# Optimization experiments

Hardware: AMD Instinct MI355X
Metric: run time of the kernel (lower is better)

Reference implementation:

```python
import jax, jax.numpy as jnp
import numpy as np

TAU = 0.01
WEIGHT = 1.0
N = 4096


def _isotonic_nondecreasing(y):
    """L2 isotonic regression: argmin_{v_1<=...<=v_n} ||v-y||^2, via the
    min-max formula v_i = max_{j<=i} min_{k>=i} mean(y[j..k]). O(n^2) but fully
    vectorized; the vjp reproduces the block-averaging Jacobian of PAV."""
    n = y.shape[0]
    cs = jnp.concatenate([jnp.zeros((1,), y.dtype), jnp.cumsum(y)])
    j = jnp.arange(n)[:, None]
    k = jnp.arange(n)[None, :]
    M = (cs[k + 1] - cs[j]) / (k - j + 1).astype(y.dtype)  # mean(y[j..k]) for j<=k
    big = jnp.asarray(jnp.inf, y.dtype)
    M = jnp.where(j <= k, M, big)
    # S[j,i] = min_{k>=i} M[j,k]  (reverse cummin along k)
    S = jax.lax.cummin(M[:, ::-1], axis=1)[:, ::-1]
    S = jnp.where(j <= k, S, -big)  # invalidate j>i before cummax over j
    T = jax.lax.cummax(S, axis=0)   # T[i,i] = max_{j<=i} S[j,i]
    return jnp.diagonal(T)


def _soft_rank(values, reg):
    """Differentiable ascending ranks via L2 projection onto the permutahedron
    of w=[n,...,1] (Blondel et al. / torchsort soft_rank, l2 regularization)."""
    n = values.shape[0]
    s_scaled = values / reg
    perm = jnp.argsort(-s_scaled)            # descending order
    s = s_scaled[perm]
    w = jnp.arange(n, 0, -1, dtype=values.dtype)
    v = -_isotonic_nondecreasing(-(s - w))
    primal = s - v
    inv = jnp.argsort(perm)
    return primal[inv]


def _soft_perm(x, tau):
    """Row-stochastic soft permutation: P[i,j] = softmax_j(-(sort(x)_i - x_j)^2/tau).
    As tau->0, P@y reorders y by ascending x."""
    xs = jnp.sort(x)
    logits = -((xs[:, None] - x[None, :]) ** 2) / tau  # [n, n]
    return jax.nn.softmax(logits, axis=-1)


def setup_inputs() -> dict:
    key = jax.random.key(0)
    k1, k2 = jax.random.split(key)
    preds = jax.random.normal(k1, (N,), dtype=jnp.float32)
    target = jax.random.normal(k2, (N,), dtype=jnp.float32)
    return {"preds": preds, "target": target}


def reference(preds, target):
    n = preds.shape[0]
    P = _soft_perm(preds, TAU)               # [n, n]
    y_sorted = P @ target                    # target soft-reordered by preds
    r_sorted = _soft_rank(y_sorted, TAU)     # soft ranks of reordered target
    diff_sum = jnp.abs(r_sorted[1:] - r_sorted[:-1]).sum()
    xi_soft = 1.0 - 3.0 * diff_sum / (n * n - 1)
    loss = -WEIGHT * xi_soft
    return loss, jax.lax.stop_gradient(xi_soft)
```

## Files before the change

kernel.cpp:

```cpp
#include <hip/hip_runtime.h>
#include <hip/hip_bf16.h>
#include <math.h>

#define N 4096


__global__ __launch_bounds__(1024, 4)
void k_A(const float* __restrict__ preds, const float* __restrict__ target,
         float* __restrict__ y) {
    __shared__ __align__(16) float4 sp4[N / 4];
    __shared__ __align__(16) float4 st4[N / 4];
    int tid = threadIdx.x;
    int b = blockIdx.x;
    int lane = tid & 63, wid = tid >> 6;
    const float4* gp = (const float4*)preds;
    const float4* gt = (const float4*)target;
    sp4[tid] = gp[tid];
    st4[tid] = gt[tid];
    __syncthreads();
    const float* sp = (const float*)sp4;
    int i0 = b * 16 + wid;
    float xv = sp[i0];
    float Z = 0.f, Nm = 0.f;
    int cnt = 0;
    #pragma unroll 4
    for (int m = 0; m < 16; m++) {
        int q = lane + 64 * m;
        float4 p4 = sp4[q];
        float4 t4 = st4[q];
        int j = q * 4;
        float d0 = xv - p4.x, d1 = xv - p4.y, d2 = xv - p4.z, d3 = xv - p4.w;
        float e0 = __expf(-100.0f * d0 * d0);
        float e1 = __expf(-100.0f * d1 * d1);
        float e2 = __expf(-100.0f * d2 * d2);
        float e3 = __expf(-100.0f * d3 * d3);
        Z += (e0 + e1) + (e2 + e3);
        Nm += e0 * t4.x + e1 * t4.y + e2 * t4.z + e3 * t4.w;
        cnt += (p4.x < xv) || (p4.x == xv && (j + 0) < i0);
        cnt += (p4.y < xv) || (p4.y == xv && (j + 1) < i0);
        cnt += (p4.z < xv) || (p4.z == xv && (j + 2) < i0);
        cnt += (p4.w < xv) || (p4.w == xv && (j + 3) < i0);
    }
    #pragma unroll
    for (int d = 32; d; d >>= 1) {
        Z += __shfl_down(Z, d);
        Nm += __shfl_down(Nm, d);
        cnt += __shfl_down(cnt, d);
    }
    if (lane == 0) y[cnt] = Nm / Z;
}

__global__ __launch_bounds__(1024, 4)
void k_B(const float* __restrict__ y, float* __restrict__ s_out,
         int* __restrict__ perm_out) {
    __shared__ __align__(16) float sy[N];
    __shared__ int part[16][65];
    int tid = threadIdx.x;
    int b = blockIdx.x;
    ((float4*)sy)[tid] = ((const float4*)y)[tid];
    __syncthreads();
    int eloc = tid & 15;
    int slice = tid >> 4;
    int i = b * 16 + eloc;
    float v = sy[i];
    int cnt = 0;
    const float4* sy4 = (const float4*)sy;
    #pragma unroll
    for (int it = 0; it < 16; it++) {
        int q = slice * 16 + ((it + slice) & 15);
        float4 a = sy4[q];
        int j = q * 4;
        cnt += (a.x > v) || (a.x == v && (j + 0) < i);
        cnt += (a.y > v) || (a.y == v && (j + 1) < i);
        cnt += (a.z > v) || (a.z == v && (j + 2) < i);
        cnt += (a.w > v) || (a.w == v && (j + 3) < i);
    }
    part[eloc][slice] = cnt;
    __syncthreads();
    if (tid < 16) {
        int r = 0;
        #pragma unroll
        for (int q = 0; q < 64; q++) r += part[tid][q];
        int i2 = b * 16 + tid;
        s_out[r] = sy[i2] * 100.0f;
        perm_out[r] = i2;
    }
}

__global__ __launch_bounds__(512, 2)
void k_C(const float* __restrict__ s, float* __restrict__ P) {
    __shared__ __align__(16) float mArr[4][512];
    __shared__ float incl[4][513];
    __shared__ double cj[16];
    __shared__ double wsum[8];
    int tid = threadIdx.x;
    int b = blockIdx.x;
    int j0 = b * 16;
    int kbase = tid * 8;
    int lane = tid & 63, wid = tid >> 6;
    double loc[8];
    {
        const float4* s4 = (const float4*)s;
        double tot = 0.0;
        #pragma unroll
        for (int q = 0; q < 2; q++) {
            float4 a = s4[tid * 2 + q];
            int t0 = kbase + q * 4;
            tot += (double)(N - (t0 + 0)) - (double)a.x; loc[q * 4 + 0] = tot;
            tot += (double)(N - (t0 + 1)) - (double)a.y; loc[q * 4 + 1] = tot;
            tot += (double)(N - (t0 + 2)) - (double)a.z; loc[q * 4 + 2] = tot;
            tot += (double)(N - (t0 + 3)) - (double)a.w; loc[q * 4 + 3] = tot;
        }
        double w = tot;
        #pragma unroll
        for (int d = 1; d < 64; d <<= 1) {
            double o = __shfl_up(w, d);
            if (lane >= d) w += o;
        }
        if (lane == 63) wsum[wid] = w;
        __syncthreads();
        double base = 0.0;
        #pragma unroll
        for (int q = 0; q < 8; q++) if (q < wid) base += wsum[q];
        double excl = base + (w - tot);
        #pragma unroll
        for (int e = 0; e < 8; e++) loc[e] += excl;
        if (tid == 2 * b) {
            cj[0] = excl;
            #pragma unroll
            for (int m = 1; m < 8; m++) cj[m] = loc[m - 1];
        }
        if (tid == 2 * b + 1) {
            cj[8] = excl;
            #pragma unroll
            for (int m = 1; m < 8; m++) cj[8 + m] = loc[m - 1];
        }
    }
    __syncthreads();
    float vloc[8];
    #pragma unroll
    for (int e = 0; e < 8; e++) vloc[e] = -INFINITY;
    float ls[4][8];
    bool live = (tid >= 2 * b);
    for (int grp = 0; grp < 4; grp++) {
        if (live) {
            #pragma unroll
            for (int rq = 0; rq < 4; rq++) {
                int j = j0 + grp * 4 + rq;
                double csj = cj[grp * 4 + rq];
                float run = INFINITY;
                #pragma unroll
                for (int e = 7; e >= 0; e--) {
                    int k = kbase + e;
                    float f = INFINITY;
                    if (k >= j) f = (float)(loc[e] - csj) * __builtin_amdgcn_rcpf((float)(k - j + 1));
                    run = fminf(f, run);
                    ls[rq][e] = run;
                }
                mArr[rq][tid] = run;
            }
        } else {
            #pragma unroll
            for (int rq = 0; rq < 4; rq++) mArr[rq][tid] = INFINITY;
        }
        __syncthreads();
        if (wid < 4) {
            const float4* mv = (const float4*)mArr[wid];
            float4 x0 = mv[2 * lane + 0];
            float4 x1 = mv[2 * lane + 1];
            float s7 = x1.w;
            float s6 = fminf(x1.z, s7);
            float s5 = fminf(x1.y, s6);
            float s4 = fminf(x1.x, s5);
            float s3 = fminf(x0.w, s4);
            float s2 = fminf(x0.z, s3);
            float s1 = fminf(x0.y, s2);
            float s0 = fminf(x0.x, s1);
            float t = s0;
            #pragma unroll
            for (int d = 1; d < 64; d <<= 1) {
                float o = __shfl_down(t, d);
                if (lane + d < 64) t = fminf(t, o);
            }
            float after = __shfl_down(t, 1);
            if (lane == 63) after = INFINITY;
            incl[wid][8 * lane + 0] = fminf(s0, after);
            incl[wid][8 * lane + 1] = fminf(s1, after);
            incl[wid][8 * lane + 2] = fminf(s2, after);
            incl[wid][8 * lane + 3] = fminf(s3, after);
            incl[wid][8 * lane + 4] = fminf(s4, after);
            incl[wid][8 * lane + 5] = fminf(s5, after);
            incl[wid][8 * lane + 6] = fminf(s6, after);
            incl[wid][8 * lane + 7] = fminf(s7, after);
            if (lane == 0) incl[wid][512] = INFINITY;
        }
        __syncthreads();
        if (live) {
            #pragma unroll
            for (int rq = 0; rq < 4; rq++) {
                int j = j0 + grp * 4 + rq;
                float aft = incl[rq][tid + 1];
                #pragma unroll
                for (int e = 0; e < 8; e++) {
                    int i = kbase + e;
                    float sv = fminf(ls[rq][e], aft);
                    if (i >= j) vloc[e] = fmaxf(vloc[e], sv);
                }
            }
        }
        __syncthreads();
    }
    if (tid >= 2 * b) {
        float4* P4 = (float4*)(P + (size_t)b * N);
        P4[tid * 2 + 0] = make_float4(vloc[0], vloc[1], vloc[2], vloc[3]);
        P4[tid * 2 + 1] = make_float4(vloc[4], vloc[5], vloc[6], vloc[7]);
    }
}

__global__ __launch_bounds__(1024, 4)
void k_reduce(const float* __restrict__ P, const float* __restrict__ s,
              const int* __restrict__ perm, float* __restrict__ r) {
    __shared__ float part[16][65];
    int tid = threadIdx.x;
    int col = tid & 15;
    int slice = tid >> 4;
    int blk = blockIdx.x;
    int i = blk * 16 + col;
    float m = -INFINITY;
    #pragma unroll
    for (int q = 0; q < 4; q++) {
        int bb = slice * 4 + q;
        if (bb <= blk) m = fmaxf(m, P[(size_t)bb * N + i]);
    }
    part[col][slice] = m;
    __syncthreads();
    if (tid < 16) {
        float T = -INFINITY;
        #pragma unroll
        for (int q = 0; q < 64; q++) T = fmaxf(T, part[tid][q]);
        int i2 = blk * 16 + tid;
        r[perm[i2]] = s[i2] + T;
    }
}

__global__ __launch_bounds__(1024, 4)
void k_finish2(const float* __restrict__ r, float* __restrict__ out) {
    __shared__ double red[16];
    int tid = threadIdx.x;
    const float4* r4 = (const float4*)r;
    float4 x = r4[tid];
    float extra = (tid < 1023) ? r[tid * 4 + 4] : 0.0f;
    double acc = 0.0;
    acc += fabs((double)x.y - (double)x.x);
    acc += fabs((double)x.z - (double)x.y);
    acc += fabs((double)x.w - (double)x.z);
    if (tid < 1023) acc += fabs((double)extra - (double)x.w);
    #pragma unroll
    for (int dd = 32; dd; dd >>= 1) acc += __shfl_down(acc, dd);
    if ((tid & 63) == 0) red[tid >> 6] = acc;
    __syncthreads();
    if (tid == 0) {
        double ds = 0.0;
        #pragma unroll
        for (int q = 0; q < 16; q++) ds += red[q];
        double xi = 1.0 - 3.0 * ds / ((double)N * (double)N - 1.0);
        out[0] = (float)(-1.0 * xi);
        out[1] = (float)xi;
    }
}

extern "C" void kernel_launch(void* const* d_in, const int* in_sizes, int n_in,
                              void* d_out, int out_size, void* d_ws, size_t ws_size,
                              hipStream_t stream) {
    const float* preds  = (const float*)d_in[0];
    const float* target = (const float*)d_in[1];
    float* out = (float*)d_out;

    char* ws = (char*)d_ws;
    float* y    = (float*)(ws);
    float* s    = (float*)(ws + 16384);
    int*   perm = (int*)(ws + 32768);
    float* r    = (float*)(ws + 49152);
    float* P    = (float*)(ws + 81920);

    k_A<<<256, 1024, 0, stream>>>(preds, target, y);
    k_B<<<256, 1024, 0, stream>>>(y, s, perm);
    k_C<<<256, 512, 0, stream>>>(s, P);
    k_reduce<<<256, 1024, 0, stream>>>(P, s, perm, r);
    k_finish2<<<1, 1024, 0, stream>>>(r, out);
}
```

Before: 86.02 us.

## Fuse all stages into one cooperative kernel with grid-wide syncs

Merges the five separate kernels into a single cooperative launch of 256 blocks of 1024 threads. Stages are separated by grid.sync() and share one union of LDS buffers. The isotonic stage is remapped to 1024 threads with 4 elements each, keeping the full prefix sum in shared memory through a padded index and using transposed scratch arrays. This removes four kernel-launch gaps and inter-kernel drain. The cost is grid-barrier overhead, a large shared-memory footprint that limits occupancy, and reliance on all 256 blocks being co-resident.

```diff
diff --git a/kernel.cpp b/kernel.cpp
--- a/kernel.cpp
+++ b/kernel.cpp
@@ -1,271 +1,258 @@
 #include <hip/hip_runtime.h>
-#include <hip/hip_bf16.h>
+#include <hip/hip_cooperative_groups.h>
 #include <math.h>
 
 #define N 4096
 
+namespace cg = cooperative_groups;
+
+
+#define CSIDX(t) ((t) + ((t) >> 4))
+
+union SharedU {
+    struct { float4 sp4[N / 4]; float4 st4[N / 4]; } pa;
+    struct { float sy[N]; int part[16][65]; } pb;
+    struct { double cs[4360]; float mT[4][16][68]; float iT[4][16][68];
+             double wsum[8]; } pc;
+    struct { float part[16][65]; } pd;
+    struct { float rl[N]; double red[16]; } pe;
+};
 
 __global__ __launch_bounds__(1024, 4)
-void k_A(const float* __restrict__ preds, const float* __restrict__ target,
-         float* __restrict__ y) {
-    __shared__ __align__(16) float4 sp4[N / 4];
-    __shared__ __align__(16) float4 st4[N / 4];
+void k_fused(const float* __restrict__ preds, const float* __restrict__ target,
+             float* __restrict__ y, float* __restrict__ s, int* __restrict__ perm,
+             float* __restrict__ P, float* __restrict__ r, float* __restrict__ out) {
+    cg::grid_group grid = cg::this_grid();
+    __shared__ SharedU sh;
     int tid = threadIdx.x;
     int b = blockIdx.x;
     int lane = tid & 63, wid = tid >> 6;
-    const float4* gp = (const float4*)preds;
-    const float4* gt = (const float4*)target;
-    sp4[tid] = gp[tid];
-    st4[tid] = gt[tid];
-    __syncthreads();
-    const float* sp = (const float*)sp4;
-    int i0 = b * 16 + wid;
-    float xv = sp[i0];
-    float Z = 0.f, Nm = 0.f;
-    int cnt = 0;
-    #pragma unroll 4
-    for (int m = 0; m < 16; m++) {
-        int q = lane + 64 * m;
-        float4 p4 = sp4[q];
-        float4 t4 = st4[q];
-        int j = q * 4;
-        float d0 = xv - p4.x, d1 = xv - p4.y, d2 = xv - p4.z, d3 = xv - p4.w;
-        float e0 = __expf(-100.0f * d0 * d0);
-        float e1 = __expf(-100.0f * d1 * d1);
-        float e2 = __expf(-100.0f * d2 * d2);
-        float e3 = __expf(-100.0f * d3 * d3);
-        Z += (e0 + e1) + (e2 + e3);
-        Nm += e0 * t4.x + e1 * t4.y + e2 * t4.z + e3 * t4.w;
-        cnt += (p4.x < xv) || (p4.x == xv && (j + 0) < i0);
-        cnt += (p4.y < xv) || (p4.y == xv && (j + 1) < i0);
-        cnt += (p4.z < xv) || (p4.z == xv && (j + 2) < i0);
-        cnt += (p4.w < xv) || (p4.w == xv && (j + 3) < i0);
-    }
-    #pragma unroll
-    for (int d = 32; d; d >>= 1) {
-        Z += __shfl_down(Z, d);
-        Nm += __shfl_down(Nm, d);
-        cnt += __shfl_down(cnt, d);
-    }
-    if (lane == 0) y[cnt] = Nm / Z;
-}
-
-__global__ __launch_bounds__(1024, 4)
-void k_B(const float* __restrict__ y, float* __restrict__ s_out,
-         int* __restrict__ perm_out) {
-    __shared__ __align__(16) float sy[N];
-    __shared__ int part[16][65];
-    int tid = threadIdx.x;
-    int b = blockIdx.x;
-    ((float4*)sy)[tid] = ((const float4*)y)[tid];
-    __syncthreads();
-    int eloc = tid & 15;
-    int slice = tid >> 4;
-    int i = b * 16 + eloc;
-    float v = sy[i];
-    int cnt = 0;
-    const float4* sy4 = (const float4*)sy;
-    #pragma unroll
-    for (int it = 0; it < 16; it++) {
-        int q = slice * 16 + ((it + slice) & 15);
-        float4 a = sy4[q];
-        int j = q * 4;
-        cnt += (a.x > v) || (a.x == v && (j + 0) < i);
-        cnt += (a.y > v) || (a.y == v && (j + 1) < i);
-        cnt += (a.z > v) || (a.z == v && (j + 2) < i);
-        cnt += (a.w > v) || (a.w == v && (j + 3) < i);
-    }
-    part[eloc][slice] = cnt;
-    __syncthreads();
-    if (tid < 16) {
-        int r = 0;
-        #pragma unroll
-        for (int q = 0; q < 64; q++) r += part[tid][q];
-        int i2 = b * 16 + tid;
-        s_out[r] = sy[i2] * 100.0f;
-        perm_out[r] = i2;
-    }
-}
-
-__global__ __launch_bounds__(512, 2)
-void k_C(const float* __restrict__ s, float* __restrict__ P) {
-    __shared__ __align__(16) float mArr[4][512];
-    __shared__ float incl[4][513];
-    __shared__ double cj[16];
-    __shared__ double wsum[8];
-    int tid = threadIdx.x;
-    int b = blockIdx.x;
-    int j0 = b * 16;
-    int kbase = tid * 8;
-    int lane = tid & 63, wid = tid >> 6;
-    double loc[8];
-    {
-        const float4* s4 = (const float4*)s;
-        double tot = 0.0;
-        #pragma unroll
-        for (int q = 0; q < 2; q++) {
-            float4 a = s4[tid * 2 + q];
-            int t0 = kbase + q * 4;
-            tot += (double)(N - (t0 + 0)) - (double)a.x; loc[q * 4 + 0] = tot;
-            tot += (double)(N - (t0 + 1)) - (double)a.y; loc[q * 4 + 1] = tot;
-            tot += (double)(N - (t0 + 2)) - (double)a.z; loc[q * 4 + 2] = tot;
-            tot += (double)(N - (t0 + 3)) - (double)a.w; loc[q * 4 + 3] = tot;
-        }
-        double w = tot;
-        #pragma unroll
-        for (int d = 1; d < 64; d <<= 1) {
-            double o = __shfl_up(w, d);
-            if (lane >= d) w += o;
-        }
-        if (lane == 63) wsum[wid] = w;
-        __syncthreads();
-        double base = 0.0;
-        #pragma unroll
-        for (int q = 0; q < 8; q++) if (q < wid) base += wsum[q];
-        double excl = base + (w - tot);
-        #pragma unroll
-        for (int e = 0; e < 8; e++) loc[e] += excl;
-        if (tid == 2 * b) {
-            cj[0] = excl;
-            #pragma unroll
-            for (int m = 1; m < 8; m++) cj[m] = loc[m - 1];
-        }
-        if (tid == 2 * b + 1) {
-            cj[8] = excl;
-            #pragma unroll
-            for (int m = 1; m < 8; m++) cj[8 + m] = loc[m - 1];
-        }
-    }
-    __syncthreads();
-    float vloc[8];
-    #pragma unroll
-    for (int e = 0; e < 8; e++) vloc[e] = -INFINITY;
-    float ls[4][8];
-    bool live = (tid >= 2 * b);
-    for (int grp = 0; grp < 4; grp++) {
-        if (live) {
-            #pragma unroll
-            for (int rq = 0; rq < 4; rq++) {
-                int j = j0 + grp * 4 + rq;
-                double csj = cj[grp * 4 + rq];
-                float run = INFINITY;
-                #pragma unroll
-                for (int e = 7; e >= 0; e--) {
-                    int k = kbase + e;
-                    float f = INFINITY;
-                    if (k >= j) f = (float)(loc[e] - csj) * __builtin_amdgcn_rcpf((float)(k - j + 1));
-                    run = fminf(f, run);
-                    ls[rq][e] = run;
-                }
-                mArr[rq][tid] = run;
-            }
-        } else {
-            #pragma unroll
-            for (int rq = 0; rq < 4; rq++) mArr[rq][tid] = INFINITY;
-        }
-        __syncthreads();
-        if (wid < 4) {
-            const float4* mv = (const float4*)mArr[wid];
-            float4 x0 = mv[2 * lane + 0];
-            float4 x1 = mv[2 * lane + 1];
-            float s7 = x1.w;
-            float s6 = fminf(x1.z, s7);
-            float s5 = fminf(x1.y, s6);
-            float s4 = fminf(x1.x, s5);
-            float s3 = fminf(x0.w, s4);
-            float s2 = fminf(x0.z, s3);
-            float s1 = fminf(x0.y, s2);
-            float s0 = fminf(x0.x, s1);
-            float t = s0;
+
+    {
+        sh.pa.sp4[tid] = ((const float4*)preds)[tid];
+        sh.pa.st4[tid] = ((const float4*)target)[tid];
+        __syncthreads();
+        const float* sp = (const float*)sh.pa.sp4;
+        int i0 = b * 16 + wid;
+        float xv = sp[i0];
+        float Z = 0.f, Nm = 0.f;
+        int cnt = 0;
+        #pragma unroll 4
+        for (int m = 0; m < 16; m++) {
+            int q = lane + 64 * m;
+            float4 p4 = sh.pa.sp4[q];
+            float4 t4 = sh.pa.st4[q];
+            int j = q * 4;
+            float d0 = xv - p4.x, d1 = xv - p4.y, d2 = xv - p4.z, d3 = xv - p4.w;
+            float e0 = __expf(-100.0f * d0 * d0);
+            float e1 = __expf(-100.0f * d1 * d1);
+            float e2 = __expf(-100.0f * d2 * d2);
+            float e3 = __expf(-100.0f * d3 * d3);
+            Z += (e0 + e1) + (e2 + e3);
+            Nm += e0 * t4.x + e1 * t4.y + e2 * t4.z + e3 * t4.w;
+            cnt += (p4.x < xv) || (p4.x == xv && (j + 0) < i0);
+            cnt += (p4.y < xv) || (p4.y == xv && (j + 1) < i0);
+            cnt += (p4.z < xv) || (p4.z == xv && (j + 2) < i0);
+            cnt += (p4.w < xv) || (p4.w == xv && (j + 3) < i0);
+        }
+        #pragma unroll
+        for (int d = 32; d; d >>= 1) {
+            Z += __shfl_down(Z, d);
+            Nm += __shfl_down(Nm, d);
+            cnt += __shfl_down(cnt, d);
+        }
+        if (lane == 0) y[cnt] = Nm / Z;
+    }
+    grid.sync();
+
+    {
+        ((float4*)sh.pb.sy)[tid] = ((const float4*)y)[tid];
+        __syncthreads();
+        int eloc = tid & 15;
+        int slice = tid >> 4;
+        int i = b * 16 + eloc;
+        float v = sh.pb.sy[i];
+        int cnt = 0;
+        const float4* sy4 = (const float4*)sh.pb.sy;
+        #pragma unroll
+        for (int it = 0; it < 16; it++) {
+            int q = slice * 16 + ((it + slice) & 15);
+            float4 a = sy4[q];
+            int j = q * 4;
+            cnt += (a.x > v) || (a.x == v && (j + 0) < i);
+            cnt += (a.y > v) || (a.y == v && (j + 1) < i);
+            cnt += (a.z > v) || (a.z == v && (j + 2) < i);
+            cnt += (a.w > v) || (a.w == v && (j + 3) < i);
+        }
+        sh.pb.part[eloc][slice] = cnt;
+        __syncthreads();
+        if (tid < 16) {
+            int rr = 0;
+            #pragma unroll
+            for (int q = 0; q < 64; q++) rr += sh.pb.part[tid][q];
+            int i2 = b * 16 + tid;
+            s[rr] = sh.pb.sy[i2] * 100.0f;
+            perm[rr] = i2;
+        }
+    }
+    grid.sync();
+
+    {
+        double tot = 0.0, wv = 0.0;
+        double loc8[8];
+        if (tid < 512) {
+            const float4* s4 = (const float4*)s;
+            #pragma unroll
+            for (int q = 0; q < 2; q++) {
+                float4 a = s4[tid * 2 + q];
+                int t0 = tid * 8 + q * 4;
+                tot += (double)(N - (t0 + 0)) - (double)a.x; loc8[q * 4 + 0] = tot;
+                tot += (double)(N - (t0 + 1)) - (double)a.y; loc8[q * 4 + 1] = tot;
+                tot += (double)(N - (t0 + 2)) - (double)a.z; loc8[q * 4 + 2] = tot;
+                tot += (double)(N - (t0 + 3)) - (double)a.w; loc8[q * 4 + 3] = tot;
+            }
+            wv = tot;
             #pragma unroll
             for (int d = 1; d < 64; d <<= 1) {
-                float o = __shfl_down(t, d);
-                if (lane + d < 64) t = fminf(t, o);
-            }
-            float after = __shfl_down(t, 1);
-            if (lane == 63) after = INFINITY;
-            incl[wid][8 * lane + 0] = fminf(s0, after);
-            incl[wid][8 * lane + 1] = fminf(s1, after);
-            incl[wid][8 * lane + 2] = fminf(s2, after);
-            incl[wid][8 * lane + 3] = fminf(s3, after);
-            incl[wid][8 * lane + 4] = fminf(s4, after);
-            incl[wid][8 * lane + 5] = fminf(s5, after);
-            incl[wid][8 * lane + 6] = fminf(s6, after);
-            incl[wid][8 * lane + 7] = fminf(s7, after);
-            if (lane == 0) incl[wid][512] = INFINITY;
-        }
-        __syncthreads();
-        if (live) {
-            #pragma unroll
-            for (int rq = 0; rq < 4; rq++) {
-                int j = j0 + grp * 4 + rq;
-                float aft = incl[rq][tid + 1];
-                #pragma unroll
-                for (int e = 0; e < 8; e++) {
-                    int i = kbase + e;
-                    float sv = fminf(ls[rq][e], aft);
-                    if (i >= j) vloc[e] = fmaxf(vloc[e], sv);
-                }
-            }
-        }
-        __syncthreads();
-    }
-    if (tid >= 2 * b) {
-        float4* P4 = (float4*)(P + (size_t)b * N);
-        P4[tid * 2 + 0] = make_float4(vloc[0], vloc[1], vloc[2], vloc[3]);
-        P4[tid * 2 + 1] = make_float4(vloc[4], vloc[5], vloc[6], vloc[7]);
-    }
-}
-
-__global__ __launch_bounds__(1024, 4)
-void k_reduce(const float* __restrict__ P, const float* __restrict__ s,
-              const int* __restrict__ perm, float* __restrict__ r) {
-    __shared__ float part[16][65];
-    int tid = threadIdx.x;
-    int col = tid & 15;
-    int slice = tid >> 4;
-    int blk = blockIdx.x;
-    int i = blk * 16 + col;
-    float m = -INFINITY;
-    #pragma unroll
-    for (int q = 0; q < 4; q++) {
-        int bb = slice * 4 + q;
-        if (bb <= blk) m = fmaxf(m, P[(size_t)bb * N + i]);
-    }
-    part[col][slice] = m;
-    __syncthreads();
-    if (tid < 16) {
-        float T = -INFINITY;
-        #pragma unroll
-        for (int q = 0; q < 64; q++) T = fmaxf(T, part[tid][q]);
-        int i2 = blk * 16 + tid;
-        r[perm[i2]] = s[i2] + T;
-    }
-}
-
-__global__ __launch_bounds__(1024, 4)
-void k_finish2(const float* __restrict__ r, float* __restrict__ out) {
-    __shared__ double red[16];
-    int tid = threadIdx.x;
-    const float4* r4 = (const float4*)r;
-    float4 x = r4[tid];
-    float extra = (tid < 1023) ? r[tid * 4 + 4] : 0.0f;
-    double acc = 0.0;
-    acc += fabs((double)x.y - (double)x.x);
-    acc += fabs((double)x.z - (double)x.y);
-    acc += fabs((double)x.w - (double)x.z);
-    if (tid < 1023) acc += fabs((double)extra - (double)x.w);
-    #pragma unroll
-    for (int dd = 32; dd; dd >>= 1) acc += __shfl_down(acc, dd);
-    if ((tid & 63) == 0) red[tid >> 6] = acc;
-    __syncthreads();
-    if (tid == 0) {
-        double ds = 0.0;
-        #pragma unroll
-        for (int q = 0; q < 16; q++) ds += red[q];
-        double xi = 1.0 - 3.0 * ds / ((double)N * (double)N - 1.0);
-        out[0] = (float)(-1.0 * xi);
-        out[1] = (float)xi;
+                double o = __shfl_up(wv, d);
+                if (lane >= d) wv += o;
+            }
+            if (lane == 63) sh.pc.wsum[wid] = wv;
+        }
+        __syncthreads();
+        if (tid < 512) {
+            double base = 0.0;
+            #pragma unroll
+            for (int q = 0; q < 8; q++) if (q < wid) base += sh.pc.wsum[q];
+            double excl = base + (wv - tot);
+            if (tid == 0) sh.pc.cs[CSIDX(0)] = 0.0;
+            #pragma unroll
+            for (int e = 0; e < 8; e++)
+                sh.pc.cs[CSIDX(tid * 8 + 1 + e)] = loc8[e] + excl;
+        }
+        __syncthreads();
+
+        int kbase = tid * 4;
+        int j0 = b * 16;
+        double kloc[4];
+        #pragma unroll
+        for (int e = 0; e < 4; e++) kloc[e] = sh.pc.cs[CSIDX(kbase + 1 + e)];
+        float vloc[4];
+        #pragma unroll
+        for (int e = 0; e < 4; e++) vloc[e] = -INFINITY;
+        float ls[4][4];
+        bool live = (tid >= 4 * b);
+        int ce = tid & 15, ct = tid >> 4;
+        for (int grp = 0; grp < 4; grp++) {
+            if (live) {
+                #pragma unroll
+                for (int rq = 0; rq < 4; rq++) {
+                    int j = j0 + grp * 4 + rq;
+                    double csj = sh.pc.cs[CSIDX(j)];
+                    float run = INFINITY;
+                    #pragma unroll
+                    for (int e = 3; e >= 0; e--) {
+                        int k = kbase + e;
+                        float f = INFINITY;
+                        if (k >= j) f = (float)(kloc[e] - csj) * __builtin_amdgcn_rcpf((float)(k - j + 1));
+                        run = fminf(f, run);
+                        ls[rq][e] = run;
+                    }
+                    sh.pc.mT[rq][ce][ct] = run;
+                }
+            } else {
+                #pragma unroll
+                for (int rq = 0; rq < 4; rq++) sh.pc.mT[rq][ce][ct] = INFINITY;
+            }
+            __syncthreads();
+            if (wid < 4) {
+                float sfx[16];
+                {
+                    float runm = INFINITY;
+                    #pragma unroll
+                    for (int e = 15; e >= 0; e--) {
+                        runm = fminf(sh.pc.mT[wid][e][lane], runm);
+                        sfx[e] = runm;
+                    }
+                }
+                float t = sfx[0];
+                #pragma unroll
+                for (int d = 1; d < 64; d <<= 1) {
+                    float o = __shfl_down(t, d);
+                    if (lane + d < 64) t = fminf(t, o);
+                }
+                float after = __shfl_down(t, 1);
+                if (lane == 63) after = INFINITY;
+                #pragma unroll
+                for (int e = 0; e < 16; e++)
+                    sh.pc.iT[wid][e][lane] = fminf(sfx[e], after);
+                if (lane == 63) sh.pc.iT[wid][0][64] = INFINITY;
+            }
+            __syncthreads();
+            if (live) {
+                int nc = tid + 1;
+                #pragma unroll
+                for (int rq = 0; rq < 4; rq++) {
+                    int j = j0 + grp * 4 + rq;
+                    float aft = sh.pc.iT[rq][nc & 15][nc >> 4];
+                    #pragma unroll
+                    for (int e = 0; e < 4; e++) {
+                        int i = kbase + e;
+                        float sv = fminf(ls[rq][e], aft);
+                        if (i >= j) vloc[e] = fmaxf(vloc[e], sv);
+                    }
+                }
+            }
+            __syncthreads();
+        }
+        if (live)
+            ((float4*)(P + (size_t)b * N))[tid] =
+                make_float4(vloc[0], vloc[1], vloc[2], vloc[3]);
+    }
+    grid.sync();
+
+    {
+        int col = tid & 15;
+        int slice = tid >> 4;
+        int i = b * 16 + col;
+        float m = -INFINITY;
+        #pragma unroll
+        for (int q = 0; q < 4; q++) {
+            int bb = slice * 4 + q;
+            if (bb <= b) m = fmaxf(m, P[(size_t)bb * N + i]);
+        }
+        sh.pd.part[col][slice] = m;
+        __syncthreads();
+        if (tid < 16) {
+            float T = -INFINITY;
+            #pragma unroll
+            for (int q = 0; q < 64; q++) T = fmaxf(T, sh.pd.part[tid][q]);
+            int i2 = b * 16 + tid;
+            r[perm[i2]] = s[i2] + T;
+        }
+    }
+    grid.sync();
+
+    if (b == 0) {
+        float4 x = ((const float4*)r)[tid];
+        float extra = (tid < 1023) ? r[tid * 4 + 4] : 0.0f;
+        double acc = 0.0;
+        acc += fabs((double)x.y - (double)x.x);
+        acc += fabs((double)x.z - (double)x.y);
+        acc += fabs((double)x.w - (double)x.z);
+        if (tid < 1023) acc += fabs((double)extra - (double)x.w);
+        #pragma unroll
+        for (int dd = 32; dd; dd >>= 1) acc += __shfl_down(acc, dd);
+        if ((tid & 63) == 0) sh.pe.red[tid >> 6] = acc;
+        __syncthreads();
+        if (tid == 0) {
+            double ds = 0.0;
+            #pragma unroll
+            for (int q = 0; q < 16; q++) ds += sh.pe.red[q];
+            double xi = 1.0 - 3.0 * ds / ((double)N * (double)N - 1.0);
+            out[0] = (float)(-1.0 * xi);
+            out[1] = (float)xi;
+        }
     }
 }
 
@@ -283,9 +270,8 @@
     float* r    = (float*)(ws + 49152);
     float* P    = (float*)(ws + 81920);
 
-    k_A<<<256, 1024, 0, stream>>>(preds, target, y);
-    k_B<<<256, 1024, 0, stream>>>(y, s, perm);
-    k_C<<<256, 512, 0, stream>>>(s, P);
-    k_reduce<<<256, 1024, 0, stream>>>(P, s, perm, r);
-    k_finish2<<<1, 1024, 0, stream>>>(r, out);
+    void* kargs[] = {(void*)&preds, (void*)&target, (void*)&y, (void*)&s,
+                     (void*)&perm, (void*)&P, (void*)&r, (void*)&out};
+    hipLaunchCooperativeKernel((const void*)k_fused, dim3(256), dim3(1024),
+                               kargs, 0, stream);
 }
```

After: 195.9 us. 2.28x slower.

## Widen isotonic kernel to 1024 threads with 4 elements each and transposed scan

Applied to the files above, without the earlier changes.

The isotonic min-max kernel now runs 1024 threads per block, each owning 4 columns instead of 8, so each thread has a shorter serial chain and there are more waves per block. The full prefix sum is stored in padded shared memory, so every thread reads its own values and the per-row cumsum from there instead of keeping a private 16-entry table. The block-level suffix-min is rewritten over a transposed 16x64 shared layout so that 4 waves each scan 16 elements per lane. The cost is extra shared-memory traffic, a larger double array in LDS, and more threads contending on each barrier.

```diff
diff --git a/kernel.cpp b/kernel.cpp
--- a/kernel.cpp
+++ b/kernel.cpp
@@ -1,9 +1,10 @@
 #include <hip/hip_runtime.h>
-#include <hip/hip_bf16.h>
 #include <math.h>
 
 #define N 4096
 
+
+#define CSIDX(t) ((t) + ((t) >> 4))
 
 __global__ __launch_bounds__(1024, 4)
 void k_A(const float* __restrict__ preds, const float* __restrict__ target,
@@ -13,10 +14,8 @@
     int tid = threadIdx.x;
     int b = blockIdx.x;
     int lane = tid & 63, wid = tid >> 6;
-    const float4* gp = (const float4*)preds;
-    const float4* gt = (const float4*)target;
-    sp4[tid] = gp[tid];
-    st4[tid] = gt[tid];
+    sp4[tid] = ((const float4*)preds)[tid];
+    st4[tid] = ((const float4*)target)[tid];
     __syncthreads();
     const float* sp = (const float*)sp4;
     int i0 = b * 16 + wid;
@@ -63,19 +62,19 @@
     int slice = tid >> 4;
     int i = b * 16 + eloc;
     float v = sy[i];
-    int cnt = 0;
+    int c = 0;
     const float4* sy4 = (const float4*)sy;
     #pragma unroll
     for (int it = 0; it < 16; it++) {
         int q = slice * 16 + ((it + slice) & 15);
         float4 a = sy4[q];
         int j = q * 4;
-        cnt += (a.x > v) || (a.x == v && (j + 0) < i);
-        cnt += (a.y > v) || (a.y == v && (j + 1) < i);
-        cnt += (a.z > v) || (a.z == v && (j + 2) < i);
-        cnt += (a.w > v) || (a.w == v && (j + 3) < i);
-    }
-    part[eloc][slice] = cnt;
+        c += (a.x > v) || (a.x == v && (j + 0) < i);
+        c += (a.y > v) || (a.y == v && (j + 1) < i);
+        c += (a.z > v) || (a.z == v && (j + 2) < i);
+        c += (a.w > v) || (a.w == v && (j + 3) < i);
+    }
+    part[eloc][slice] = c;
     __syncthreads();
     if (tid < 16) {
         int r = 0;
@@ -87,96 +86,94 @@
     }
 }
 
-__global__ __launch_bounds__(512, 2)
+__global__ __launch_bounds__(1024, 4)
 void k_C(const float* __restrict__ s, float* __restrict__ P) {
-    __shared__ __align__(16) float mArr[4][512];
-    __shared__ float incl[4][513];
-    __shared__ double cj[16];
+    __shared__ double cs[4360];
+    __shared__ float mT[4][16][68];
+    __shared__ float iT[4][16][68];
     __shared__ double wsum[8];
     int tid = threadIdx.x;
     int b = blockIdx.x;
-    int j0 = b * 16;
-    int kbase = tid * 8;
     int lane = tid & 63, wid = tid >> 6;
-    double loc[8];
-    {
+
+    double tot = 0.0, wv = 0.0;
+    double loc8[8];
+    if (tid < 512) {
         const float4* s4 = (const float4*)s;
-        double tot = 0.0;
         #pragma unroll
         for (int q = 0; q < 2; q++) {
             float4 a = s4[tid * 2 + q];
-            int t0 = kbase + q * 4;
-            tot += (double)(N - (t0 + 0)) - (double)a.x; loc[q * 4 + 0] = tot;
-            tot += (double)(N - (t0 + 1)) - (double)a.y; loc[q * 4 + 1] = tot;
-            tot += (double)(N - (t0 + 2)) - (double)a.z; loc[q * 4 + 2] = tot;
-            tot += (double)(N - (t0 + 3)) - (double)a.w; loc[q * 4 + 3] = tot;
-        }
-        double w = tot;
+            int t0 = tid * 8 + q * 4;
+            tot += (double)(N - (t0 + 0)) - (double)a.x; loc8[q * 4 + 0] = tot;
+            tot += (double)(N - (t0 + 1)) - (double)a.y; loc8[q * 4 + 1] = tot;
+            tot += (double)(N - (t0 + 2)) - (double)a.z; loc8[q * 4 + 2] = tot;
+            tot += (double)(N - (t0 + 3)) - (double)a.w; loc8[q * 4 + 3] = tot;
+        }
+        wv = tot;
         #pragma unroll
         for (int d = 1; d < 64; d <<= 1) {
-            double o = __shfl_up(w, d);
-            if (lane >= d) w += o;
-        }
-        if (lane == 63) wsum[wid] = w;
-        __syncthreads();
+            double o = __shfl_up(wv, d);
+            if (lane >= d) wv += o;
+        }
+        if (lane == 63) wsum[wid] = wv;
+    }
+    __syncthreads();
+    if (tid < 512) {
         double base = 0.0;
         #pragma unroll
         for (int q = 0; q < 8; q++) if (q < wid) base += wsum[q];
-        double excl = base + (w - tot);
-        #pragma unroll
-        for (int e = 0; e < 8; e++) loc[e] += excl;
-        if (tid == 2 * b) {
-            cj[0] = excl;
-            #pragma unroll
-            for (int m = 1; m < 8; m++) cj[m] = loc[m - 1];
-        }
-        if (tid == 2 * b + 1) {
-            cj[8] = excl;
-            #pragma unroll
-            for (int m = 1; m < 8; m++) cj[8 + m] = loc[m - 1];
-        }
-    }
-    __syncthreads();
-    float vloc[8];
-    #pragma unroll
-    for (int e = 0; e < 8; e++) vloc[e] = -INFINITY;
-    float ls[4][8];
-    bool live = (tid >= 2 * b);
+        double excl = base + (wv - tot);
+        if (tid == 0) cs[CSIDX(0)] = 0.0;
+        #pragma unroll
+        for (int e = 0; e < 8; e++)
+            cs[CSIDX(tid * 8 + 1 + e)] = loc8[e] + excl;
+    }
+    __syncthreads();
+
+    int kbase = tid * 4;
+    int j0 = b * 16;
+    double kloc[4];
+    #pragma unroll
+    for (int e = 0; e < 4; e++) kloc[e] = cs[CSIDX(kbase + 1 + e)];
+    float vloc[4];
+    #pragma unroll
+    for (int e = 0; e < 4; e++) vloc[e] = -INFINITY;
+    float ls[4][4];
+    bool live = (tid >= 4 * b);
+    int ce = tid & 15, ct = tid >> 4;
     for (int grp = 0; grp < 4; grp++) {
         if (live) {
             #pragma unroll
             for (int rq = 0; rq < 4; rq++) {
                 int j = j0 + grp * 4 + rq;
-                double csj = cj[grp * 4 + rq];
+                double csj = cs[CSIDX(j)];
                 float run = INFINITY;
                 #pragma unroll
-                for (int e = 7; e >= 0; e--) {
+                for (int e = 3; e >= 0; e--) {
                     int k = kbase + e;
                     float f = INFINITY;
-                    if (k >= j) f = (float)(loc[e] - csj) * __builtin_amdgcn_rcpf((float)(k - j + 1));
+                    if (k >= j) f = (float)(kloc[e] - csj) * __builtin_amdgcn_rcpf((float)(k - j + 1));
                     run = fminf(f, run);
                     ls[rq][e] = run;
                 }
-                mArr[rq][tid] = run;
+                mT[rq][ce][ct] = run;
             }
         } else {
             #pragma unroll
-            for (int rq = 0; rq < 4; rq++) mArr[rq][tid] = INFINITY;
+            for (int rq = 0; rq < 4; rq++) mT[rq][ce][ct] = INFINITY;
         }
         __syncthreads();
         if (wid < 4) {
-            const float4* mv = (const float4*)mArr[wid];
-            float4 x0 = mv[2 * lane + 0];
-            float4 x1 = mv[2 * lane + 1];
-            float s7 = x1.w;
-            float s6 = fminf(x1.z, s7);
-            float s5 = fminf(x1.y, s6);
-            float s4 = fminf(x1.x, s5);
-            float s3 = fminf(x0.w, s4);
-            float s2 = fminf(x0.z, s3);
-            float s1 = fminf(x0.y, s2);
-            float s0 = fminf(x0.x, s1);
-            float t = s0;
+            float sfx[16];
+            {
+                float runm = INFINITY;
+                #pragma unroll
+                for (int e = 15; e >= 0; e--) {
+                    runm = fminf(mT[wid][e][lane], runm);
+                    sfx[e] = runm;
+                }
+            }
+            float t = sfx[0];
             #pragma unroll
             for (int d = 1; d < 64; d <<= 1) {
                 float o = __shfl_down(t, d);
@@ -184,24 +181,20 @@
             }
             float after = __shfl_down(t, 1);
             if (lane == 63) after = INFINITY;
-            incl[wid][8 * lane + 0] = fminf(s0, after);
-            incl[wid][8 * lane + 1] = fminf(s1, after);
-            incl[wid][8 * lane + 2] = fminf(s2, after);
-            incl[wid][8 * lane + 3] = fminf(s3, after);
-            incl[wid][8 * lane + 4] = fminf(s4, after);
-            incl[wid][8 * lane + 5] = fminf(s5, after);
-            incl[wid][8 * lane + 6] = fminf(s6, after);
-            incl[wid][8 * lane + 7] = fminf(s7, after);
-            if (lane == 0) incl[wid][512] = INFINITY;
+            #pragma unroll
+            for (int e = 0; e < 16; e++)
+                iT[wid][e][lane] = fminf(sfx[e], after);
+            if (lane == 63) iT[wid][0][64] = INFINITY;
         }
         __syncthreads();
         if (live) {
+            int nc = tid + 1;
             #pragma unroll
             for (int rq = 0; rq < 4; rq++) {
                 int j = j0 + grp * 4 + rq;
-                float aft = incl[rq][tid + 1];
+                float aft = iT[rq][nc & 15][nc >> 4];
                 #pragma unroll
-                for (int e = 0; e < 8; e++) {
+                for (int e = 0; e < 4; e++) {
                     int i = kbase + e;
                     float sv = fminf(ls[rq][e], aft);
                     if (i >= j) vloc[e] = fmaxf(vloc[e], sv);
@@ -210,11 +203,9 @@
         }
         __syncthreads();
     }
-    if (tid >= 2 * b) {
-        float4* P4 = (float4*)(P + (size_t)b * N);
-        P4[tid * 2 + 0] = make_float4(vloc[0], vloc[1], vloc[2], vloc[3]);
-        P4[tid * 2 + 1] = make_float4(vloc[4], vloc[5], vloc[6], vloc[7]);
-    }
+    if (live)
+        ((float4*)(P + (size_t)b * N))[tid] =
+            make_float4(vloc[0], vloc[1], vloc[2], vloc[3]);
 }
 
 __global__ __launch_bounds__(1024, 4)
@@ -285,7 +276,7 @@
 
     k_A<<<256, 1024, 0, stream>>>(preds, target, y);
     k_B<<<256, 1024, 0, stream>>>(y, s, perm);
-    k_C<<<256, 512, 0, stream>>>(s, P);
+    k_C<<<256, 1024, 0, stream>>>(s, P);
     k_reduce<<<256, 1024, 0, stream>>>(P, s, perm, r);
     k_finish2<<<1, 1024, 0, stream>>>(r, out);
 }
```

Result: no change. 87.31 us (+1.5%).
